# Kernel tuning notes

Measured on AMD Instinct MI355X. Metric: run time of the kernel, lower is better.

The kernel has to match this reference:

```python
import jax, jax.numpy as jnp
import numpy as np

V_IN = 32000
V_OUT = 32000
E = 1024
H = 1024
B = 16
T = 512


def _lstm_layer(xs, Wih, Whh, bih, bhh):
    # xs: [T, B, in_dim]; PyTorch gate order: i, f, g, o (each size H)
    gx = jnp.einsum('tbi,gi->tbg', xs, Wih) + bih + bhh  # [T, B, 4H]

    def step(carry, g_t):
        h, c = carry
        g = g_t + h @ Whh.T  # [B, 4H]
        i, f, gg, o = jnp.split(g, 4, axis=-1)
        i = jax.nn.sigmoid(i)
        f = jax.nn.sigmoid(f)
        gg = jnp.tanh(gg)
        o = jax.nn.sigmoid(o)
        c = f * c + i * gg
        h = o * jnp.tanh(c)
        return (h, c), h

    h0 = jnp.zeros((xs.shape[1], Whh.shape[1]), dtype=xs.dtype)
    c0 = jnp.zeros_like(h0)
    _, hs = jax.lax.scan(step, (h0, c0), gx)
    return hs  # [T, B, H]


def setup_inputs() -> dict:
    key = jax.random.key(0)
    ks = jax.random.split(key, 12)
    s_e = 1.0  # nn.Embedding default init is N(0,1)
    s_l = 1.0 / np.sqrt(H)  # LSTM/Linear uniform bound 1/sqrt(H)

    def u(k, shape):
        return jax.random.uniform(k, shape, jnp.float32, -s_l, s_l)

    return {
        'x': jax.random.randint(ks[0], (B, T), 0, V_IN),
        'emb': jax.random.normal(ks[1], (V_IN, E), jnp.float32) * s_e,
        'W_ih0': u(ks[2], (4 * H, E)),
        'W_hh0': u(ks[3], (4 * H, H)),
        'b_ih0': u(ks[4], (4 * H,)),
        'b_hh0': u(ks[5], (4 * H,)),
        'W_ih1': u(ks[6], (4 * H, H)),
        'W_hh1': u(ks[7], (4 * H, H)),
        'b_ih1': u(ks[8], (4 * H,)),
        'b_hh1': u(ks[9], (4 * H,)),
        'W_out': u(ks[10], (V_OUT, H)),
        'b_out': u(ks[11], (V_OUT,)),
    }


def reference(x, emb, W_ih0, W_hh0, b_ih0, b_hh0, W_ih1, W_hh1, b_ih1, b_hh1, W_out, b_out):
    # embedding + permute to [T, B, E]
    out = emb[x].transpose(1, 0, 2)
    out = _lstm_layer(out, W_ih0, W_hh0, b_ih0, b_hh0)
    out = _lstm_layer(out, W_ih1, W_hh1, b_ih1, b_hh1)
    logits = jnp.einsum('tbh,oh->tbo', out, W_out) + b_out
    return logits.transpose(1, 0, 2)  # [B, T, V_OUT]
```

## Files before the change

kernel.cpp:

```cpp
#include <hip/hip_runtime.h>
#include <cstdint>
#include <cstddef>

typedef __bf16 bf16;
typedef float f32x4 __attribute__((ext_vector_type(4)));
typedef bf16 bf16x8 __attribute__((ext_vector_type(8)));

#define AS1 __attribute__((address_space(1)))
#define AS3 __attribute__((address_space(3)))

__device__ __forceinline__ void gload_lds16(const void* g, void* l) {
  __builtin_amdgcn_global_load_lds((AS1 void*)g, (AS3 void*)l, 16, 0, 0);
}

#define FLAG_WORDS 1024

__global__ __launch_bounds__(256) void init_misc(
    const float* __restrict__ bih0, const float* __restrict__ bhh0,
    const float* __restrict__ bih1, const float* __restrict__ bhh1,
    float* __restrict__ bsum0, float* __restrict__ bsum1, unsigned* __restrict__ flags) {
  int i = blockIdx.x * 256 + threadIdx.x;
  if (i < 4096) {
    bsum0[i] = bih0[i] + bhh0[i];
    bsum1[i] = bih1[i] + bhh1[i];
  }
  if (i < FLAG_WORDS) flags[i] = 0u;
}

__global__ __launch_bounds__(256) void gemm_emb(
    const int* __restrict__ x, const float* __restrict__ emb,
    const float* __restrict__ Wih0, const float* __restrict__ bsum0,
    float* __restrict__ C, const float* __restrict__ Wout, bf16* __restrict__ woutb) {
  if (blockIdx.x >= 2048) {
    size_t base = ((size_t)(blockIdx.x - 2048) * 8192) + (size_t)threadIdx.x * 8;
    if (woutb) {
      for (int it = 0; it < 4; ++it) {
        size_t i = base + (size_t)it * 2048;
        f32x4 v0 = *(const f32x4*)(Wout + i);
        f32x4 v1 = *(const f32x4*)(Wout + i + 4);
        bf16x8 r;
        for (int j = 0; j < 4; ++j) { r[j] = (bf16)v0[j]; r[j + 4] = (bf16)v1[j]; }
        *(bf16x8*)(woutb + i) = r;
      }
    }
    return;
  }
  __shared__ bf16 aL[2][4096];
  __shared__ bf16 bL[2][4096];
  const int tid = threadIdx.x;
  const int l = tid & 63, w = tid >> 6;
  const int bm = blockIdx.x & 63;
  const int bn = blockIdx.x >> 6;
  const int wr = (w >> 1) << 6, wc = (w & 1) << 6;
  const int r16 = l & 15, kq = l >> 4;

  f32x4 acc[4][4];
  for (int m = 0; m < 4; ++m)
    for (int n = 0; n < 4; ++n) acc[m][n] = (f32x4){0.f, 0.f, 0.f, 0.f};

  auto stage = [&](int kt, int buf) {
    for (int i = 0; i < 2; ++i) {
      int lin = tid + (i << 8);
      int r = lin >> 2, c = lin & 3;
      int rg = (bm << 7) + r;
      int tok = x[((rg & 15) << 9) + (rg >> 4)];
      const float* sa = emb + ((size_t)tok << 10) + (kt << 5) + (c << 3);
      f32x4 a0 = *(const f32x4*)sa;
      f32x4 a1 = *(const f32x4*)(sa + 4);
      bf16x8 oa;
      for (int j = 0; j < 4; ++j) { oa[j] = (bf16)a0[j]; oa[j + 4] = (bf16)a1[j]; }
      *(bf16x8*)&aL[buf][(r << 5) + ((c ^ (r & 3)) << 3)] = oa;
      const float* sb = Wih0 + (size_t)((bn << 7) + r) * 1024 + (kt << 5) + (c << 3);
      f32x4 b0 = *(const f32x4*)sb;
      f32x4 b1 = *(const f32x4*)(sb + 4);
      bf16x8 ob;
      for (int j = 0; j < 4; ++j) { ob[j] = (bf16)b0[j]; ob[j + 4] = (bf16)b1[j]; }
      *(bf16x8*)&bL[buf][(r << 5) + ((c ^ (r & 3)) << 3)] = ob;
    }
  };
  stage(0, 0);
  __syncthreads();
  for (int kt = 0; kt < 32; ++kt) {
    int cur = kt & 1;
    if (kt + 1 < 32) stage(kt + 1, cur ^ 1);
    bf16x8 af[4], bfr[4];
    for (int m = 0; m < 4; ++m) {
      int row = wr + (m << 4) + r16;
      int ch = kq ^ (row & 3);
      af[m] = *(const bf16x8*)&aL[cur][(row << 5) + (ch << 3)];
    }
    for (int n = 0; n < 4; ++n) {
      int row = wc + (n << 4) + r16;
      int ch = kq ^ (row & 3);
      bfr[n] = *(const bf16x8*)&bL[cur][(row << 5) + (ch << 3)];
    }
    for (int m = 0; m < 4; ++m)
      for (int n = 0; n < 4; ++n)
        acc[m][n] = __builtin_amdgcn_mfma_f32_16x16x32_bf16(af[m], bfr[n], acc[m][n], 0, 0, 0);
    __syncthreads();
  }
  float bvv[4];
  for (int n = 0; n < 4; ++n) bvv[n] = bsum0[(bn << 7) + wc + (n << 4) + r16];
  for (int m = 0; m < 4; ++m) {
    int Rbase = (bm << 7) + wr + (m << 4) + (kq << 2);
    for (int r = 0; r < 4; ++r) {
      int R = Rbase + r;
      size_t rowoff = (size_t)R * 4096;
      for (int n = 0; n < 4; ++n)
        C[rowoff + (bn << 7) + wc + (n << 4) + r16] = acc[m][n][r] + bvv[n];
    }
  }
}

template <bool BF16B>
__global__ __launch_bounds__(256) void gemm_proj(
    const bf16* __restrict__ A, const void* __restrict__ Bw_,
    const float* __restrict__ bias, float* __restrict__ C) {
  __shared__ bf16 aL[2][4096];
  __shared__ bf16 bL[2][4096];
  const int tid = threadIdx.x;
  const int l = tid & 63, w = tid >> 6;
  const int k = blockIdx.x % 80, sq = blockIdx.x / 80;
  const int bm = ((sq & 7) << 3) + (k & 7);
  const int bn = (sq >> 3) * 10 + (k >> 3);
  const int wr = (w >> 1) << 6, wc = (w & 1) << 6;
  const int r16 = l & 15, kq = l >> 4;
  const bf16* Bb = (const bf16*)Bw_;
  const float* Bf32 = (const float*)Bw_;

  f32x4 acc[4][4];
  for (int m = 0; m < 4; ++m)
    for (int n = 0; n < 4; ++n) acc[m][n] = (f32x4){0.f, 0.f, 0.f, 0.f};

  auto stageA = [&](int kt, int buf) {
    for (int i = 0; i < 2; ++i) {
      int lin = tid + (i << 8);
      int r = lin >> 2, s = lin & 3, c = s ^ (r & 3);
      gload_lds16(A + (size_t)((bm << 7) + r) * 1024 + (kt << 5) + (c << 3),
                  &aL[buf][lin << 3]);
    }
  };
  stageA(0, 0);
  if (BF16B) {
    for (int i = 0; i < 2; ++i) {
      int lin = tid + (i << 8);
      int r = lin >> 2, s = lin & 3, c = s ^ (r & 3);
      gload_lds16(Bb + (size_t)((bn << 7) + r) * 1024 + (c << 3), &bL[0][lin << 3]);
    }
  } else {
    for (int i = 0; i < 2; ++i) {
      int lin = tid + (i << 8);
      int r = lin >> 2, c = lin & 3;
      const float* src = Bf32 + (size_t)((bn << 7) + r) * 1024 + (c << 3);
      f32x4 v0 = *(const f32x4*)src;
      f32x4 v1 = *(const f32x4*)(src + 4);
      bf16x8 o;
      for (int j = 0; j < 4; ++j) { o[j] = (bf16)v0[j]; o[j + 4] = (bf16)v1[j]; }
      *(bf16x8*)&bL[0][(r << 5) + ((c ^ (r & 3)) << 3)] = o;
    }
  }
  __syncthreads();

  for (int kt = 0; kt < 32; ++kt) {
    const int cur = kt & 1;
    const bool pf = (kt + 1 < 32);
    f32x4 bv0[2], bv1[2];
    int br_[2], bs_[2];
    if (pf) {
      stageA(kt + 1, cur ^ 1);
      if (BF16B) {
        for (int i = 0; i < 2; ++i) {
          int lin = tid + (i << 8);
          int r = lin >> 2, s = lin & 3, c = s ^ (r & 3);
          gload_lds16(Bb + (size_t)((bn << 7) + r) * 1024 + ((kt + 1) << 5) + (c << 3),
                      &bL[cur ^ 1][lin << 3]);
        }
      } else {
        for (int i = 0; i < 2; ++i) {
          int lin = tid + (i << 8);
          int r = lin >> 2, c = lin & 3;
          const float* src = Bf32 + (size_t)((bn << 7) + r) * 1024 + ((kt + 1) << 5) + (c << 3);
          bv0[i] = *(const f32x4*)src;
          bv1[i] = *(const f32x4*)(src + 4);
          br_[i] = r;
          bs_[i] = c ^ (r & 3);
        }
      }
    }
    bf16x8 af[4], bfr[4];
    for (int m = 0; m < 4; ++m) {
      int row = wr + (m << 4) + r16;
      int ch = kq ^ (row & 3);
      af[m] = *(const bf16x8*)&aL[cur][(row << 5) + (ch << 3)];
    }
    for (int n = 0; n < 4; ++n) {
      int row = wc + (n << 4) + r16;
      int ch = kq ^ (row & 3);
      bfr[n] = *(const bf16x8*)&bL[cur][(row << 5) + (ch << 3)];
    }
    for (int m = 0; m < 4; ++m)
      for (int n = 0; n < 4; ++n)
        acc[m][n] = __builtin_amdgcn_mfma_f32_16x16x32_bf16(af[m], bfr[n], acc[m][n], 0, 0, 0);
    if (pf && !BF16B) {
      for (int i = 0; i < 2; ++i) {
        bf16x8 o;
        for (int j = 0; j < 4; ++j) { o[j] = (bf16)bv0[i][j]; o[j + 4] = (bf16)bv1[i][j]; }
        *(bf16x8*)&bL[cur ^ 1][(br_[i] << 5) + (bs_[i] << 3)] = o;
      }
    }
    __syncthreads();
  }

  float bvv[4];
  for (int n = 0; n < 4; ++n) bvv[n] = bias[(bn << 7) + wc + (n << 4) + r16];
  for (int m = 0; m < 4; ++m) {
    int Rbase = (bm << 7) + wr + (m << 4) + (kq << 2);
    for (int r = 0; r < 4; ++r) {
      int R = Rbase + r;
      int tt = R >> 4, bb = R & 15;
      size_t rowoff = ((size_t)bb * 512 + tt) * 32000;
      for (int n = 0; n < 4; ++n) {
        float v = acc[m][n][r] + bvv[n];
        float* cp = &C[rowoff + (bn << 7) + wc + (n << 4) + r16];
        asm volatile("global_store_dword %0, %1, off nt" ::"v"(cp), "v"(v) : "memory");
      }
    }
  }
}

__global__ __launch_bounds__(256, 1) void lstm_pipe3(
    const float* __restrict__ gx,
    const float* __restrict__ Whh0,
    const float* __restrict__ Wih1,
    const float* __restrict__ Whh1,
    const float* __restrict__ bsum1,
    bf16* __restrict__ hs0t,
    bf16* __restrict__ hs1t,
    float* __restrict__ gx1,
    bf16* __restrict__ hs1rm,
    unsigned* __restrict__ flags,
    int T) {
  __shared__ bf16 wlds[4][16 * 1024];
  __shared__ unsigned short hb[4][64];
  __shared__ unsigned tokv[4];
  const int tid = threadIdx.x;
  const int l = tid & 63, w = tid >> 6;
  const int bid = blockIdx.x;
  const int r16 = l & 15, kq = l >> 4;
  unsigned* const fL0 = flags;
  unsigned* const fB = flags + 256;
  unsigned* const fL1 = flags + 512;
  const int typ = bid >> 6;
  const int lb = bid & 63;
  const int widx = lb * 4 + w;
  const int colbase = lb * 16 + w * 4;

  {
    const float* Wsrc = (typ == 0) ? Whh0 : ((typ == 1) ? Wih1 : Whh1);
    for (int it = 0; it < 32; ++it) {
      int lin = it * 64 + l;
      int row = lin >> 7, cs = lin & 127, c = cs ^ (row & 7);
      const float* s = Wsrc + (size_t)((row >> 2) * 1024 + colbase + (row & 3)) * 1024 + c * 8;
      f32x4 v0 = *(const f32x4*)s;
      f32x4 v1 = *(const f32x4*)(s + 4);
      bf16x8 o;
      for (int j = 0; j < 4; ++j) { o[j] = (bf16)v0[j]; o[j + 4] = (bf16)v1[j]; }
      *(bf16x8*)&wlds[w][row * 1024 + cs * 8] = o;
    }
  }
  if (tid < 4) tokv[tid] = 0;
  __syncthreads();

  const int gcol = (r16 >> 2) * 1024 + colbase + (r16 & 3);
  const int b0s = (r16 >> 2) & 1, b1s = (r16 >> 3) & 1;

  auto pollq = [&](unsigned* arr, unsigned tgt) {
    unsigned* q = arr + w * 64 + (l & 15) * 4;
    for (;;) {
      unsigned a0 = __hip_atomic_load(q + 0, __ATOMIC_RELAXED, __HIP_MEMORY_SCOPE_AGENT);
      unsigned a1 = __hip_atomic_load(q + 1, __ATOMIC_RELAXED, __HIP_MEMORY_SCOPE_AGENT);
      unsigned a2 = __hip_atomic_load(q + 2, __ATOMIC_RELAXED, __HIP_MEMORY_SCOPE_AGENT);
      unsigned a3 = __hip_atomic_load(q + 3, __ATOMIC_RELAXED, __HIP_MEMORY_SCOPE_AGENT);
      if (__all(a0 >= tgt && a1 >= tgt && a2 >= tgt && a3 >= tgt)) break;
      __builtin_amdgcn_s_sleep(2);
    }
    volatile unsigned* tk = tokv;
    if (l == 0) tk[w] = tgt;
    while (tk[0] < tgt || tk[1] < tgt || tk[2] < tgt || tk[3] < tgt) {
    }
    asm volatile("" ::: "memory");
  };
  auto poll1 = [&](unsigned* p, unsigned tgt) {
    while (__hip_atomic_load(p, __ATOMIC_RELAXED, __HIP_MEMORY_SCOPE_AGENT) < tgt)
      __builtin_amdgcn_s_sleep(2);
    asm volatile("" ::: "memory");
  };
  auto chain = [&](const bf16* plane) -> f32x4 {
    f32x4 acc = (f32x4){0.f, 0.f, 0.f, 0.f};
    const char* hp = (const char*)plane;
#pragma unroll 8
    for (int kk = 0; kk < 32; ++kk) {
      int tl = kk * 8 + kq * 2;
      unsigned long long lo = *(const unsigned long long*)(hp + tl * 128 + r16 * 8);
      unsigned long long hi = *(const unsigned long long*)(hp + tl * 128 + 128 + r16 * 8);
      union { struct { unsigned long long a, b; } u; bf16x8 v; } A;
      A.u.a = lo;
      A.u.b = hi;
      bf16x8 Bf = *(const bf16x8*)&wlds[w][r16 * 1024 + (((kk * 4 + kq) ^ (r16 & 7)) << 3)];
      acc = __builtin_amdgcn_mfma_f32_16x16x32_bf16(A.v, Bf, acc, 0, 0, 0);
    }
    return acc;
  };

  if (typ == 1) {
    const float bsv = bsum1[gcol];
    unsigned* const myflag = fB + widx;
    for (int t = 0; t < T; ++t) {
      pollq(fL0, (unsigned)(t + 1));
      f32x4 acc = chain(hs0t + (size_t)t * 16384);
      for (int r = 0; r < 4; ++r) acc[r] += bsv;
      float* dst = gx1 + (size_t)t * 65536 + widx * 256 + r16 * 16 + kq * 4;
      asm volatile("global_store_dwordx4 %0, %1, off sc0 sc1" ::"v"(dst), "v"(acc) : "memory");
      asm volatile("s_waitcnt vmcnt(0)" ::: "memory");
      if (l == 0)
        __hip_atomic_store(myflag, (unsigned)(t + 1), __ATOMIC_RELAXED, __HIP_MEMORY_SCOPE_AGENT);
    }
    return;
  }

  float cst[4] = {0.f, 0.f, 0.f, 0.f};
  unsigned* const myflag = (typ == 0) ? (fL0 + widx) : (fL1 + widx);
  unsigned* const bpartner = fB + widx;
  bf16* const houts = (typ == 0) ? hs0t : hs1t;

  for (int t = 0; t < T; ++t) {
    f32x4 acc = (f32x4){0.f, 0.f, 0.f, 0.f};
    f32x4 g1;
    if (typ == 0) {
      float gxv[4];
      for (int r = 0; r < 4; ++r)
        gxv[r] = gx[(size_t)(t * 16 + kq * 4 + r) * 4096 + gcol];
      if (t > 0) pollq(fL0, (unsigned)t);
      if (t > 0) acc = chain(houts + (size_t)(t - 1) * 16384);
      for (int r = 0; r < 4; ++r) acc[r] += gxv[r];
    } else {
      poll1(bpartner, (unsigned)(t + 1));
      const float* gp = gx1 + (size_t)t * 65536 + widx * 256 + r16 * 16 + kq * 4;
      asm volatile("global_load_dwordx4 %0, %1, off sc0 sc1" : "=v"(g1) : "v"(gp) : "memory");
      if (t > 0) pollq(fL1, (unsigned)t);
      if (t > 0) acc = chain(houts + (size_t)(t - 1) * 16384);
      asm volatile("s_waitcnt vmcnt(0)" ::: "memory");
      __builtin_amdgcn_sched_barrier(0);
      for (int r = 0; r < 4; ++r) acc[r] += g1[r];
    }
    float hv[4];
    for (int r = 0; r < 4; ++r) {
      float own = acc[r];
      float p4 = __shfl_xor(own, 4, 64);
      float ev = b0s ? p4 : own;
      float ov = b0s ? own : p4;
      float ev8 = __shfl_xor(ev, 8, 64);
      float ov8 = __shfl_xor(ov, 8, 64);
      float xi = b1s ? ev8 : ev;
      float xf = b1s ? ov8 : ov;
      float xg = b1s ? ev : ev8;
      float xo = b1s ? ov : ov8;
      float ig = 1.f / (1.f + __expf(-xi));
      float fg = 1.f / (1.f + __expf(-xf));
      float eg = __expf(2.f * xg);
      float gv = 1.f - 2.f / (eg + 1.f);
      float og = 1.f / (1.f + __expf(-xo));
      cst[r] = fg * cst[r] + ig * gv;
      float ec = __expf(2.f * cst[r]);
      float th = 1.f - 2.f / (ec + 1.f);
      hv[r] = og * th;
    }
    if (r16 < 4) {
      volatile unsigned short* hbp = hb[w];
      for (int r = 0; r < 4; ++r) {
        bf16 hbv = (bf16)hv[r];
        hbp[(kq * 4 + r) * 4 + r16] = __builtin_bit_cast(unsigned short, hbv);
      }
    }
    unsigned long long rowv = 0;
    if (l < 16) rowv = *(volatile unsigned long long*)&hb[w][l * 4];
    if (l < 16) {
      char* dst = (char*)houts + (size_t)t * 32768 + widx * 128 + l * 8;
      asm volatile("global_store_dwordx2 %0, %1, off sc0 sc1" ::"v"(dst), "v"(rowv) : "memory");
    }
    asm volatile("s_waitcnt vmcnt(0)" ::: "memory");
    if (l == 0)
      __hip_atomic_store(myflag, (unsigned)(t + 1), __ATOMIC_RELAXED, __HIP_MEMORY_SCOPE_AGENT);
    if (typ == 2 && l < 16) {
      *(unsigned long long*)((char*)hs1rm + ((size_t)(t * 16 + l) * 1024 + colbase) * 2) = rowv;
    }
  }
}

extern "C" void kernel_launch(void* const* d_in, const int* in_sizes, int n_in,
                              void* d_out, int out_size, void* d_ws, size_t ws_size,
                              hipStream_t stream) {
  const int* x = (const int*)d_in[0];
  const float* emb = (const float*)d_in[1];
  const float* Wih0 = (const float*)d_in[2];
  const float* Whh0 = (const float*)d_in[3];
  const float* bih0 = (const float*)d_in[4];
  const float* bhh0 = (const float*)d_in[5];
  const float* Wih1 = (const float*)d_in[6];
  const float* Whh1 = (const float*)d_in[7];
  const float* bih1 = (const float*)d_in[8];
  const float* bhh1 = (const float*)d_in[9];
  const float* Wout = (const float*)d_in[10];
  const float* bout = (const float*)d_in[11];

  const int T = 512, M = 8192;
  const size_t bfb = (size_t)M * 1024 * 2;
  const size_t out_bytes = (size_t)out_size * 4;
  const size_t woutb_bytes = (size_t)32000 * 1024 * 2;

  char* p = (char*)d_ws;
  bf16* hs1rm = (bf16*)p;         p += bfb;
  float* bsum0 = (float*)p;       p += 4096 * 4;
  float* bsum1 = (float*)p;       p += 4096 * 4;
  unsigned* flags = (unsigned*)p; p += FLAG_WORDS * 4;
  size_t base_need = (size_t)(p - (char*)d_ws);
  const bool fat = ws_size >= base_need + woutb_bytes + 256;
  bf16* woutb = fat ? (bf16*)p : nullptr;

  float* gx = (float*)d_out;
  float* gx1 = (float*)((char*)d_out + (512ull << 20));
  char* tail = (char*)d_out + out_bytes - 2 * bfb;
  bf16* hs0t = (bf16*)tail;
  bf16* hs1t = (bf16*)(tail + bfb);

  init_misc<<<64, 256, 0, stream>>>(bih0, bhh0, bih1, bhh1, bsum0, bsum1, flags);
  gemm_emb<<<2048 + 4000, 256, 0, stream>>>(x, emb, Wih0, bsum0, gx, Wout, woutb);
  lstm_pipe3<<<192, 256, 0, stream>>>(gx, Whh0, Wih1, Whh1, bsum1, hs0t, hs1t, gx1, hs1rm,
                                      flags, T);
  if (fat)
    gemm_proj<true><<<16000, 256, 0, stream>>>(hs1rm, woutb, bout, (float*)d_out);
  else
    gemm_proj<false><<<16000, 256, 0, stream>>>(hs1rm, Wout, bout, (float*)d_out);
}
```

Baseline: 5.306 ms.

## Use ring buffer for layer-1 input gates and hoist GEMM staging address math

The producer wavefronts that compute layer-1 input projections now write into an 8-slot ring buffer instead of a full T-length array. A backpressure poll on the consumer's flag keeps the producer at most RING steps ahead. The consumer loads the ring slot after the recurrent chain, with its wait fused into the load. Separately, the embedding GEMM precomputes per-thread row pointers and LDS offsets once instead of recomputing the token gather every k-tile. The ring is meant to keep gx1 resident in cache, but it couples producer and consumer more tightly and makes the gx1 load serial after the chain rather than overlapped with it.

```diff
diff --git a/kernel.cpp b/kernel.cpp
--- a/kernel.cpp
+++ b/kernel.cpp
@@ -13,6 +13,7 @@
   __builtin_amdgcn_global_load_lds((AS1 void*)g, (AS3 void*)l, 16, 0, 0);
 }
 
+#define RING 8
 #define FLAG_WORDS 1024
 
 __global__ __launch_bounds__(256) void init_misc(
@@ -54,28 +55,37 @@
   const int wr = (w >> 1) << 6, wc = (w & 1) << 6;
   const int r16 = l & 15, kq = l >> 4;
 
+  const float* embrow[2];
+  const float* wrow[2];
+  int sdst[2];
+  for (int i = 0; i < 2; ++i) {
+    int lin = tid + (i << 8);
+    int r = lin >> 2, c = lin & 3;
+    int rg = (bm << 7) + r;
+    int tok = x[((rg & 15) << 9) + (rg >> 4)];
+    embrow[i] = emb + ((size_t)tok << 10) + (c << 3);
+    wrow[i] = Wih0 + (size_t)((bn << 7) + r) * 1024 + (c << 3);
+    sdst[i] = (r << 5) + ((c ^ (r & 3)) << 3);
+  }
+
   f32x4 acc[4][4];
   for (int m = 0; m < 4; ++m)
     for (int n = 0; n < 4; ++n) acc[m][n] = (f32x4){0.f, 0.f, 0.f, 0.f};
 
   auto stage = [&](int kt, int buf) {
     for (int i = 0; i < 2; ++i) {
-      int lin = tid + (i << 8);
-      int r = lin >> 2, c = lin & 3;
-      int rg = (bm << 7) + r;
-      int tok = x[((rg & 15) << 9) + (rg >> 4)];
-      const float* sa = emb + ((size_t)tok << 10) + (kt << 5) + (c << 3);
+      const float* sa = embrow[i] + (kt << 5);
       f32x4 a0 = *(const f32x4*)sa;
       f32x4 a1 = *(const f32x4*)(sa + 4);
       bf16x8 oa;
       for (int j = 0; j < 4; ++j) { oa[j] = (bf16)a0[j]; oa[j + 4] = (bf16)a1[j]; }
-      *(bf16x8*)&aL[buf][(r << 5) + ((c ^ (r & 3)) << 3)] = oa;
-      const float* sb = Wih0 + (size_t)((bn << 7) + r) * 1024 + (kt << 5) + (c << 3);
+      *(bf16x8*)&aL[buf][sdst[i]] = oa;
+      const float* sb = wrow[i] + (kt << 5);
       f32x4 b0 = *(const f32x4*)sb;
       f32x4 b1 = *(const f32x4*)(sb + 4);
       bf16x8 ob;
       for (int j = 0; j < 4; ++j) { ob[j] = (bf16)b0[j]; ob[j + 4] = (bf16)b1[j]; }
-      *(bf16x8*)&bL[buf][(r << 5) + ((c ^ (r & 3)) << 3)] = ob;
+      *(bf16x8*)&bL[buf][sdst[i]] = ob;
     }
   };
   stage(0, 0);
@@ -315,11 +325,13 @@
   if (typ == 1) {
     const float bsv = bsum1[gcol];
     unsigned* const myflag = fB + widx;
+    unsigned* const partner = fL1 + widx;
     for (int t = 0; t < T; ++t) {
+      if (t >= RING) poll1(partner, (unsigned)(t - RING + 1));
       pollq(fL0, (unsigned)(t + 1));
       f32x4 acc = chain(hs0t + (size_t)t * 16384);
       for (int r = 0; r < 4; ++r) acc[r] += bsv;
-      float* dst = gx1 + (size_t)t * 65536 + widx * 256 + r16 * 16 + kq * 4;
+      float* dst = gx1 + (size_t)(t & (RING - 1)) * 65536 + widx * 256 + r16 * 16 + kq * 4;
       asm volatile("global_store_dwordx4 %0, %1, off sc0 sc1" ::"v"(dst), "v"(acc) : "memory");
       asm volatile("s_waitcnt vmcnt(0)" ::: "memory");
       if (l == 0)
@@ -334,23 +346,26 @@
   bf16* const houts = (typ == 0) ? hs0t : hs1t;
 
   for (int t = 0; t < T; ++t) {
-    f32x4 acc = (f32x4){0.f, 0.f, 0.f, 0.f};
-    f32x4 g1;
+    float gxv[4];
     if (typ == 0) {
-      float gxv[4];
       for (int r = 0; r < 4; ++r)
         gxv[r] = gx[(size_t)(t * 16 + kq * 4 + r) * 4096 + gcol];
+    }
+    if (typ == 0) {
       if (t > 0) pollq(fL0, (unsigned)t);
-      if (t > 0) acc = chain(houts + (size_t)(t - 1) * 16384);
+    } else {
+      poll1(bpartner, (unsigned)(t + 1));
+      if (t > 0) pollq(fL1, (unsigned)t);
+    }
+    f32x4 acc = (f32x4){0.f, 0.f, 0.f, 0.f};
+    if (t > 0) acc = chain(houts + (size_t)(t - 1) * 16384);
+    if (typ == 0) {
       for (int r = 0; r < 4; ++r) acc[r] += gxv[r];
     } else {
-      poll1(bpartner, (unsigned)(t + 1));
-      const float* gp = gx1 + (size_t)t * 65536 + widx * 256 + r16 * 16 + kq * 4;
-      asm volatile("global_load_dwordx4 %0, %1, off sc0 sc1" : "=v"(g1) : "v"(gp) : "memory");
-      if (t > 0) pollq(fL1, (unsigned)t);
-      if (t > 0) acc = chain(houts + (size_t)(t - 1) * 16384);
-      asm volatile("s_waitcnt vmcnt(0)" ::: "memory");
-      __builtin_amdgcn_sched_barrier(0);
+      const float* gp = gx1 + (size_t)(t & (RING - 1)) * 65536 + widx * 256 + r16 * 16 + kq * 4;
+      f32x4 g1;
+      asm volatile("global_load_dwordx4 %0, %1, off sc0 sc1\ns_waitcnt vmcnt(0)"
+                   : "=v"(g1) : "v"(gp) : "memory");
       for (int r = 0; r < 4; ++r) acc[r] += g1[r];
     }
     float hv[4];
```

New measurement: 4.999 ms. -5.8%, faster.
